# Kernel tuning notes

Measured on AMD Instinct MI355X. Metric: run time of the kernel, lower is better.

The kernel has to match this reference:

```python
import jax, jax.numpy as jnp
import numpy as np
from jax import lax

B, T = 16384, 10
H = 256
CAR_V, REG_V, POI_V, WEEK_V, TIME_V = 1000000, 100000, 1000, 7, 1440
LABELS = 500
IN = 39  # 16+8+4+3+8


def _lstm_layer(x, Wih, Whh, bih, bhh):
    # x: [B, T, D] -> outputs [B, T, H]; PyTorch gate order i,f,g,o
    b = x.shape[0]
    h0 = jnp.zeros((b, H), x.dtype)
    c0 = jnp.zeros((b, H), x.dtype)
    # Precompute input projections for all timesteps in one GEMM
    xg = jnp.einsum('btd,gd->btg', x, Wih) + bih + bhh  # [B, T, 4H]

    def step(carry, xt_g):
        h, c = carry
        gates = xt_g + h @ Whh.T  # [B, 4H]
        i, f, g, o = jnp.split(gates, 4, axis=-1)
        i, f, o = jax.nn.sigmoid(i), jax.nn.sigmoid(f), jax.nn.sigmoid(o)
        g = jnp.tanh(g)
        c = f * c + i * g
        h = o * jnp.tanh(c)
        return (h, c), h

    _, ys = lax.scan(step, (h0, c0), xg.transpose(1, 0, 2))  # ys: [T, B, H]
    return ys.transpose(1, 0, 2)


def setup_inputs() -> dict:
    key = jax.random.key(0)
    ks = jax.random.split(key, 20)
    s = 0.05
    return {
        'car_idx': jax.random.randint(ks[0], (B, T), 0, CAR_V),
        'region_idx': jax.random.randint(ks[1], (B, T), 0, REG_V),
        'poi_idx': jax.random.randint(ks[2], (B, T), 0, POI_V),
        'week_idx': jax.random.randint(ks[3], (B, T), 0, WEEK_V),
        'time_idx': jax.random.randint(ks[4], (B, T), 0, TIME_V),
        'car_emb': jax.random.normal(ks[5], (CAR_V, 16), jnp.float32) * s,
        'region_emb': jax.random.normal(ks[6], (REG_V, 8), jnp.float32) * s,
        'poi_emb': jax.random.normal(ks[7], (POI_V, 4), jnp.float32) * s,
        'week_emb': jax.random.normal(ks[8], (WEEK_V, 3), jnp.float32) * s,
        'time_emb': jax.random.normal(ks[9], (TIME_V, 8), jnp.float32) * s,
        'Wih0': jax.random.normal(ks[10], (4 * H, IN), jnp.float32) * s,
        'Whh0': jax.random.normal(ks[11], (4 * H, H), jnp.float32) * s,
        'bih0': jax.random.normal(ks[12], (4 * H,), jnp.float32) * s,
        'bhh0': jax.random.normal(ks[13], (4 * H,), jnp.float32) * s,
        'Wih1': jax.random.normal(ks[14], (4 * H, H), jnp.float32) * s,
        'Whh1': jax.random.normal(ks[15], (4 * H, H), jnp.float32) * s,
        'bih1': jax.random.normal(ks[16], (4 * H,), jnp.float32) * s,
        'bhh1': jax.random.normal(ks[17], (4 * H,), jnp.float32) * s,
        'Wout': jax.random.normal(ks[18], (LABELS, H), jnp.float32) * s,
        'bout': jax.random.normal(ks[19], (LABELS,), jnp.float32) * s,
    }


def reference(car_idx, region_idx, poi_idx, week_idx, time_idx,
              car_emb, region_emb, poi_emb, week_emb, time_emb,
              Wih0, Whh0, bih0, bhh0, Wih1, Whh1, bih1, bhh1,
              Wout, bout):
    # Batched version of the original per-item embedding-lookup + concat loop
    x = jnp.concatenate([
        car_emb[car_idx],      # [B, T, 16]
        region_emb[region_idx],  # [B, T, 8]
        poi_emb[poi_idx],      # [B, T, 4]
        week_emb[week_idx],    # [B, T, 3]
        time_emb[time_idx],    # [B, T, 8]
    ], axis=-1)  # [B, T, 39]
    h1 = _lstm_layer(x, Wih0, Whh0, bih0, bhh0)
    h2 = _lstm_layer(h1, Wih1, Whh1, bih1, bhh1)
    return h2[:, -1, :] @ Wout.T + bout  # [B, LABELS]
```

## Files before the change

### kernel.cpp

```cpp
#include <hip/hip_runtime.h>
#include <hip/hip_bf16.h>

#define BB 16384
#define TT 10
#define NLAB 500

typedef __attribute__((ext_vector_type(8))) __bf16 bf16x8;
typedef __attribute__((ext_vector_type(4))) float f32x4;
typedef __attribute__((ext_vector_type(8))) short short8v;

__device__ __forceinline__ unsigned short f2bf(float f) {
  union { float f; unsigned int u; } x; x.f = f;
  unsigned int r = 0x7fffu + ((x.u >> 16) & 1u);
  return (unsigned short)((x.u + r) >> 16);
}

__device__ __forceinline__ float sigm(float x) {
  return __builtin_amdgcn_rcpf(1.f + __builtin_amdgcn_exp2f(-1.4426950408889634f * x));
}
__device__ __forceinline__ float tanh_(float x) {
  float ax = fabsf(x);
  float e = __builtin_amdgcn_exp2f(-2.8853900817779268f * ax);
  float r = (1.f - e) * __builtin_amdgcn_rcpf(1.f + e);
  return copysignf(r, x);
}

__device__ __forceinline__ void gload_lds16(const unsigned short* g, unsigned short* l) {
  __builtin_amdgcn_global_load_lds(
      (const __attribute__((address_space(1))) unsigned int*)g,
      (__attribute__((address_space(3))) unsigned int*)l, 16, 0, 0);
}

#define SCHED0() __builtin_amdgcn_sched_barrier(0)
#define BAR_LGKM()                                                       \
  { SCHED0(); asm volatile("s_waitcnt lgkmcnt(0)" ::: "memory");         \
    __builtin_amdgcn_s_barrier(); SCHED0(); }
#define BAR_LGKM_VM4()                                                   \
  { SCHED0(); asm volatile("s_waitcnt vmcnt(4) lgkmcnt(0)" ::: "memory");\
    __builtin_amdgcn_s_barrier(); SCHED0(); }

__global__ void prep_w(const float* __restrict__ Wih0, const float* __restrict__ Whh0,
                       const float* __restrict__ bih0, const float* __restrict__ bhh0,
                       const float* __restrict__ Wih1, const float* __restrict__ Whh1,
                       const float* __restrict__ bih1, const float* __restrict__ bhh1,
                       const float* __restrict__ Wout, const float* __restrict__ bout,
                       unsigned short* __restrict__ wall, float* __restrict__ bblob) {
  int i = blockIdx.x * 256 + threadIdx.x;
  if (i < 983040) {
    int c = i >> 14, r = i & 16383;
    int wid = r >> 11, frag = (r >> 9) & 3, lane = (r >> 3) & 63, e = r & 7;
    int kin = ((lane >> 4) << 3) + e;
    float v;
    if (c < 20) {
      int pass = c / 10, ks = c % 10;
      int n = (pass * 2 + (frag >> 1)) * 256 + wid * 32 + (frag & 1) * 16 + (lane & 15);
      int k = ks * 32 + kin;
      if (k < 64) v = (k < 39) ? Wih0[n * 39 + k] : 0.f;
      else        v = Whh0[n * 256 + (k - 64)];
    } else if (c < 52) {
      int idx = c - 20;
      int pass = idx >> 4, half = (idx >> 3) & 1, ks = idx & 7;
      int n = (pass * 2 + (frag >> 1)) * 256 + wid * 32 + (frag & 1) * 16 + (lane & 15);
      int k = ks * 32 + kin;
      v = half ? Wih1[n * 256 + k]
               : Whh1[n * 256 + k];
    } else {
      int ks = c - 52;
      int n = wid * 64 + frag * 16 + (lane & 15);
      int k = ks * 32 + kin;
      v = (n < NLAB) ? Wout[n * 256 + k] : 0.f;
    }
    wall[i] = f2bf(v);
  } else {
    int j = i - 983040;
    if (j < 1024)       bblob[j] = bih0[j] + bhh0[j];
    else if (j < 2048)  bblob[j] = bih1[j - 1024] + bhh1[j - 1024];
    else if (j < 2560) { int n = j - 2048; bblob[j] = (n < NLAB) ? bout[n] : 0.f; }
  }
}

__global__ void gather_x(const int* __restrict__ car_idx, const int* __restrict__ region_idx,
                         const int* __restrict__ poi_idx, const int* __restrict__ week_idx,
                         const int* __restrict__ time_idx,
                         const float* __restrict__ car_emb, const float* __restrict__ region_emb,
                         const float* __restrict__ poi_emb, const float* __restrict__ week_emb,
                         const float* __restrict__ time_emb,
                         unsigned short* __restrict__ xfrag) {
  int tid = blockIdx.x * 256 + threadIdx.x;
  if (tid >= BB * TT) return;
  int t = tid / BB;
  int b = tid - t * BB;
  int ii = b * TT + t;
  float v[64];
#pragma unroll
  for (int k = 0; k < 64; ++k) v[k] = 0.f;
  { const float* p = car_emb + (size_t)car_idx[ii] * 16;
#pragma unroll
    for (int k = 0; k < 16; ++k) v[k] = p[k]; }
  { const float* p = region_emb + (size_t)region_idx[ii] * 8;
#pragma unroll
    for (int k = 0; k < 8; ++k) v[16 + k] = p[k]; }
  { const float* p = poi_emb + (size_t)poi_idx[ii] * 4;
#pragma unroll
    for (int k = 0; k < 4; ++k) v[24 + k] = p[k]; }
  { const float* p = week_emb + (size_t)week_idx[ii] * 3;
#pragma unroll
    for (int k = 0; k < 3; ++k) v[28 + k] = p[k]; }
  { const float* p = time_emb + (size_t)time_idx[ii] * 8;
#pragma unroll
    for (int k = 0; k < 8; ++k) v[31 + k] = p[k]; }

  int tile = b >> 6, rb = (b >> 4) & 3, lrow = b & 15;
  size_t base = ((size_t)tile * TT + t) * 4096;
#pragma unroll
  for (int c = 0; c < 8; ++c) {
    int kc = c >> 2;
    int lane = lrow + ((c & 3) << 4);
    size_t off = base + (size_t)((((kc << 2) + rb) << 6) + lane) * 8;
    short8v s;
#pragma unroll
    for (int e = 0; e < 8; ++e) s[e] = (short)f2bf(v[c * 8 + e]);
    *(short8v*)(xfrag + off) = s;
  }
}

__device__ __forceinline__ f32x4 MF(bf16x8 a, bf16x8 b, f32x4 c) {
  return __builtin_amdgcn_mfma_f32_16x16x32_bf16(a, b, c, 0, 0, 0);
}

template <int NKS, int SPLIT>
__device__ __forceinline__ void gemm_pass(f32x4 (&acc)[2][2][4], bf16x8 (&bc)[4],
    const unsigned short* wp, const unsigned short* wnext,
    const unsigned short* ab1, const unsigned short* ab2, int lane) {
#define AADDR(KS) \
  ((SPLIT < NKS && (KS) >= SPLIT) ? (ab2 + ((KS) - SPLIT) * 2048) : (ab1 + (KS) * 2048))
  bf16x8 aA[4], aB[4];
  {
    const unsigned short* a0 = AADDR(0);
#pragma unroll
    for (int rb = 0; rb < 4; ++rb) aA[rb] = *(const bf16x8*)(a0 + rb * 512 + lane * 8);
  }
#pragma unroll 1
  for (int ks = 0; ks < NKS; ks += 2) {
    bf16x8 bn[4], b2[4];
    const unsigned short* w1 = wp + 16384;
#pragma unroll
    for (int f = 0; f < 4; ++f) bn[f] = *(const bf16x8*)(w1 + f * 512);
    const unsigned short* w2 = (ks + 2 < NKS) ? (wp + 32768) : wnext;
#pragma unroll
    for (int f = 0; f < 4; ++f) b2[f] = *(const bf16x8*)(w2 + f * 512);
    const unsigned short* an = AADDR(ks + 1);
#pragma unroll
    for (int rb = 0; rb < 4; ++rb) aB[rb] = *(const bf16x8*)(an + rb * 512 + lane * 8);
#pragma unroll
    for (int gl = 0; gl < 2; ++gl)
#pragma unroll
      for (int nb = 0; nb < 2; ++nb)
#pragma unroll
        for (int rb = 0; rb < 4; ++rb)
          acc[gl][nb][rb] = MF(aA[rb], bc[gl * 2 + nb], acc[gl][nb][rb]);
    const unsigned short* an2 = AADDR((ks + 2 < NKS) ? (ks + 2) : (NKS - 1));
#pragma unroll
    for (int rb = 0; rb < 4; ++rb) aA[rb] = *(const bf16x8*)(an2 + rb * 512 + lane * 8);
#pragma unroll
    for (int gl = 0; gl < 2; ++gl)
#pragma unroll
      for (int nb = 0; nb < 2; ++nb)
#pragma unroll
        for (int rb = 0; rb < 4; ++rb)
          acc[gl][nb][rb] = MF(aB[rb], bn[gl * 2 + nb], acc[gl][nb][rb]);
#pragma unroll
    for (int f = 0; f < 4; ++f) bc[f] = b2[f];
    wp += 32768;
  }
#undef AADDR
}

__device__ __forceinline__ void partial_if(f32x4 (&acc)[2][2][4], f32x4 (&cst)[2][4],
                                           float* sib) {
#pragma unroll
  for (int nb = 0; nb < 2; ++nb)
#pragma unroll
    for (int rb = 0; rb < 4; ++rb)
#pragma unroll
      for (int r = 0; r < 4; ++r) {
        sib[((nb << 4) + (rb << 2) + r) << 6] = sigm(acc[0][nb][rb][r]);
        cst[nb][rb][r] = sigm(acc[1][nb][rb][r]) * cst[nb][rb][r];
      }
}

__device__ __forceinline__ void finish_go(f32x4 (&acc)[2][2][4], f32x4 (&cst)[2][4],
    const float* sib, unsigned short* hbuf, int lane, int wid) {
  int lrow = ((lane >> 4) << 2);
  int l15 = lane & 15;
#pragma unroll
  for (int nb = 0; nb < 2; ++nb) {
    int jw = (nb << 4) + l15;
    int lane_dst_base = ((jw >> 3) << 4);
    int elem = jw & 7;
#pragma unroll
    for (int rb = 0; rb < 4; ++rb)
#pragma unroll
      for (int r = 0; r < 4; ++r) {
        float g = tanh_(acc[0][nb][rb][r]);
        float o = sigm(acc[1][nb][rb][r]);
        float c = cst[nb][rb][r] + sib[((nb << 4) + (rb << 2) + r) << 6] * g;
        cst[nb][rb][r] = c;
        float h = o * tanh_(c);
        int lane_dst = lrow + r + lane_dst_base;
        hbuf[(size_t)((((wid << 2) + rb) << 6) + lane_dst) * 8 + elem] = f2bf(h);
      }
  }
}

__global__ __launch_bounds__(512, 1) void lstm_fused(
    const unsigned short* __restrict__ xfrag, const unsigned short* __restrict__ wall,
    const float* __restrict__ bblob, float* __restrict__ out) {
  __shared__ __align__(16) unsigned short h1s[16384];
  __shared__ __align__(16) unsigned short h2s[16384];
  __shared__ __align__(16) unsigned short xts[4096];
  __shared__ __align__(16) float bls[2560];
  __shared__ __align__(16) float sis[16384];

  int tid = threadIdx.x, lane = tid & 63, wid = tid >> 6;
  int tile = blockIdx.x, b0 = tile << 6, l15 = lane & 15;

  { short8v z = {0, 0, 0, 0, 0, 0, 0, 0};
    short8v* p1 = (short8v*)h1s; short8v* p2 = (short8v*)h2s;
    for (int i = tid; i < 2048; i += 512) { p1[i] = z; p2[i] = z; } }
  for (int i = tid; i < 2560; i += 512) bls[i] = bblob[i];
  gload_lds16(xfrag + (size_t)(tile * TT) * 4096 + wid * 512 + lane * 8, xts + wid * 512);

  float* sib = sis + (wid << 11) + lane;

  const unsigned short* wb = wall + wid * 2048 + lane * 8;

  bf16x8 bc[4];
#pragma unroll
  for (int f = 0; f < 4; ++f) bc[f] = *(const bf16x8*)(wb + f * 512);

  asm volatile("s_waitcnt vmcnt(0)" ::: "memory");
  __syncthreads();

  f32x4 c1[2][4], c2[2][4];
#pragma unroll
  for (int nb = 0; nb < 2; ++nb)
#pragma unroll
    for (int rb = 0; rb < 4; ++rb) {
      c1[nb][rb] = (f32x4){0.f, 0.f, 0.f, 0.f};
      c2[nb][rb] = (f32x4){0.f, 0.f, 0.f, 0.f};
    }
  f32x4 acc[2][2][4];

#define ACC_BIAS(BOFF, GBASE)                                                     \
  _Pragma("unroll")                                                               \
  for (int gl = 0; gl < 2; ++gl)                                                  \
    _Pragma("unroll")                                                             \
    for (int nb = 0; nb < 2; ++nb) {                                              \
      float bv = bls[(BOFF) + (((GBASE) + gl) << 8) + (wid << 5) + (nb << 4) + l15]; \
      _Pragma("unroll")                                                           \
      for (int rb = 0; rb < 4; ++rb) acc[gl][nb][rb] = (f32x4){bv, bv, bv, bv};   \
    }

#pragma unroll 1
  for (int t = 0; t < TT; ++t) {
    ACC_BIAS(0, 0)
    gemm_pass<10, 2>(acc, bc, wb, wb + 163840, xts, h1s, lane);
    partial_if(acc, c1, sib);
    ACC_BIAS(0, 2)
    gemm_pass<10, 2>(acc, bc, wb + 163840, wb + 327680, xts, h1s, lane);
    BAR_LGKM()
    if (t < TT - 1)
      gload_lds16(xfrag + (size_t)(tile * TT + t + 1) * 4096 + wid * 512 + lane * 8,
                  xts + wid * 512);
    finish_go(acc, c1, sib, h1s, lane, wid);
    ACC_BIAS(1024, 0)
    gemm_pass<8, 8>(acc, bc, wb + 327680, wb + 458752, h2s, h2s, lane);
    BAR_LGKM()
    gemm_pass<8, 8>(acc, bc, wb + 458752, wb + 589824, h1s, h1s, lane);
    partial_if(acc, c2, sib);
    ACC_BIAS(1024, 2)
    gemm_pass<8, 8>(acc, bc, wb + 589824, wb + 720896, h2s, h2s, lane);
    gemm_pass<8, 8>(acc, bc, wb + 720896,
                    (t < TT - 1) ? wb : (wb + 851968), h1s, h1s, lane);
    BAR_LGKM_VM4()
    finish_go(acc, c2, sib, h2s, lane, wid);
  }
  BAR_LGKM()

#pragma unroll
  for (int gl = 0; gl < 2; ++gl)
#pragma unroll
    for (int nb = 0; nb < 2; ++nb) {
      float bv = bls[2048 + (wid << 6) + ((gl * 2 + nb) << 4) + l15];
#pragma unroll
      for (int rb = 0; rb < 4; ++rb) acc[gl][nb][rb] = (f32x4){bv, bv, bv, bv};
    }
  gemm_pass<8, 8>(acc, bc, wb + 851968, wb + 851968, h2s, h2s, lane);

#pragma unroll
  for (int gl = 0; gl < 2; ++gl)
#pragma unroll
    for (int nb = 0; nb < 2; ++nb) {
      int n = (wid << 6) + ((gl * 2 + nb) << 4) + l15;
      if (n < NLAB) {
#pragma unroll
        for (int rb = 0; rb < 4; ++rb)
#pragma unroll
          for (int r = 0; r < 4; ++r) {
            int row = (rb << 4) + ((lane >> 4) << 2) + r;
            out[(size_t)(b0 + row) * NLAB + n] = acc[gl][nb][rb][r];
          }
      }
    }
#undef ACC_BIAS
}

extern "C" void kernel_launch(void* const* d_in, const int* in_sizes, int n_in,
                              void* d_out, int out_size, void* d_ws, size_t ws_size,
                              hipStream_t stream) {
  const int* car_idx    = (const int*)d_in[0];
  const int* region_idx = (const int*)d_in[1];
  const int* poi_idx    = (const int*)d_in[2];
  const int* week_idx   = (const int*)d_in[3];
  const int* time_idx   = (const int*)d_in[4];
  const float* car_emb    = (const float*)d_in[5];
  const float* region_emb = (const float*)d_in[6];
  const float* poi_emb    = (const float*)d_in[7];
  const float* week_emb   = (const float*)d_in[8];
  const float* time_emb   = (const float*)d_in[9];
  const float* Wih0 = (const float*)d_in[10];
  const float* Whh0 = (const float*)d_in[11];
  const float* bih0 = (const float*)d_in[12];
  const float* bhh0 = (const float*)d_in[13];
  const float* Wih1 = (const float*)d_in[14];
  const float* Whh1 = (const float*)d_in[15];
  const float* bih1 = (const float*)d_in[16];
  const float* bhh1 = (const float*)d_in[17];
  const float* Wout = (const float*)d_in[18];
  const float* bout = (const float*)d_in[19];

  unsigned short* xfrag = (unsigned short*)d_ws;
  unsigned short* wallp = xfrag + 10485760;
  float* bblob = (float*)(wallp + 983040);

  prep_w<<<3850, 256, 0, stream>>>(Wih0, Whh0, bih0, bhh0, Wih1, Whh1, bih1, bhh1,
                                   Wout, bout, wallp, bblob);
  gather_x<<<640, 256, 0, stream>>>(car_idx, region_idx, poi_idx, week_idx, time_idx,
                                    car_emb, region_emb, poi_emb, week_emb, time_emb, xfrag);
  lstm_fused<<<256, 512, 0, stream>>>(xfrag, wallp, bblob, (float*)d_out);
}
```

Measured before the change: 299.0 us.

## Peel first timestep to skip zero-state recurrent GEMMs and tune MFMA scheduling

Peels timestep zero out of the loop. Since h1 and h2 start at zero, it runs only the input-projection GEMMs there, which skips the recurrent Whh work and the LDS zero-initialisation. The change also merges two layer-2 gate passes into one 16-step pass, loads the next B fragments directly into bc instead of through a temporary to save registers, and wraps the MFMA blocks in s_setprio. tanh is simplified to 2*sigmoid(2x)-1, which drops the abs/copysign but may overflow or lose precision for large negative inputs.

```diff
diff --git a/kernel.cpp b/kernel.cpp
--- a/kernel.cpp
+++ b/kernel.cpp
@@ -19,10 +19,8 @@
   return __builtin_amdgcn_rcpf(1.f + __builtin_amdgcn_exp2f(-1.4426950408889634f * x));
 }
 __device__ __forceinline__ float tanh_(float x) {
-  float ax = fabsf(x);
-  float e = __builtin_amdgcn_exp2f(-2.8853900817779268f * ax);
-  float r = (1.f - e) * __builtin_amdgcn_rcpf(1.f + e);
-  return copysignf(r, x);
+  float e = __builtin_amdgcn_exp2f(-2.8853900817779268f * x);
+  return 2.f * __builtin_amdgcn_rcpf(1.f + e) - 1.f;
 }
 
 __device__ __forceinline__ void gload_lds16(const unsigned short* g, unsigned short* l) {
@@ -142,16 +140,14 @@
   }
 #pragma unroll 1
   for (int ks = 0; ks < NKS; ks += 2) {
-    bf16x8 bn[4], b2[4];
+    bf16x8 bn[4];
     const unsigned short* w1 = wp + 16384;
 #pragma unroll
     for (int f = 0; f < 4; ++f) bn[f] = *(const bf16x8*)(w1 + f * 512);
-    const unsigned short* w2 = (ks + 2 < NKS) ? (wp + 32768) : wnext;
-#pragma unroll
-    for (int f = 0; f < 4; ++f) b2[f] = *(const bf16x8*)(w2 + f * 512);
     const unsigned short* an = AADDR(ks + 1);
 #pragma unroll
     for (int rb = 0; rb < 4; ++rb) aB[rb] = *(const bf16x8*)(an + rb * 512 + lane * 8);
+    __builtin_amdgcn_s_setprio(1);
 #pragma unroll
     for (int gl = 0; gl < 2; ++gl)
 #pragma unroll
@@ -159,9 +155,14 @@
 #pragma unroll
         for (int rb = 0; rb < 4; ++rb)
           acc[gl][nb][rb] = MF(aA[rb], bc[gl * 2 + nb], acc[gl][nb][rb]);
+    __builtin_amdgcn_s_setprio(0);
+    const unsigned short* w2 = (ks + 2 < NKS) ? (wp + 32768) : wnext;
+#pragma unroll
+    for (int f = 0; f < 4; ++f) bc[f] = *(const bf16x8*)(w2 + f * 512);
     const unsigned short* an2 = AADDR((ks + 2 < NKS) ? (ks + 2) : (NKS - 1));
 #pragma unroll
     for (int rb = 0; rb < 4; ++rb) aA[rb] = *(const bf16x8*)(an2 + rb * 512 + lane * 8);
+    __builtin_amdgcn_s_setprio(1);
 #pragma unroll
     for (int gl = 0; gl < 2; ++gl)
 #pragma unroll
@@ -169,8 +170,7 @@
 #pragma unroll
         for (int rb = 0; rb < 4; ++rb)
           acc[gl][nb][rb] = MF(aB[rb], bn[gl * 2 + nb], acc[gl][nb][rb]);
-#pragma unroll
-    for (int f = 0; f < 4; ++f) bc[f] = b2[f];
+    __builtin_amdgcn_s_setprio(0);
     wp += 32768;
   }
 #undef AADDR
@@ -225,9 +225,6 @@
   int tid = threadIdx.x, lane = tid & 63, wid = tid >> 6;
   int tile = blockIdx.x, b0 = tile << 6, l15 = lane & 15;
 
-  { short8v z = {0, 0, 0, 0, 0, 0, 0, 0};
-    short8v* p1 = (short8v*)h1s; short8v* p2 = (short8v*)h2s;
-    for (int i = tid; i < 2048; i += 512) { p1[i] = z; p2[i] = z; } }
   for (int i = tid; i < 2560; i += 512) bls[i] = bblob[i];
   gload_lds16(xfrag + (size_t)(tile * TT) * 4096 + wid * 512 + lane * 8, xts + wid * 512);
 
@@ -262,8 +259,26 @@
       for (int rb = 0; rb < 4; ++rb) acc[gl][nb][rb] = (f32x4){bv, bv, bv, bv};   \
     }
 
+  ACC_BIAS(0, 0)
+  gemm_pass<2, 2>(acc, bc, wb, wb + 163840, xts, xts, lane);
+  partial_if(acc, c1, sib);
+  ACC_BIAS(0, 2)
+  gemm_pass<2, 2>(acc, bc, wb + 163840, wb + 458752, xts, xts, lane);
+  BAR_LGKM()
+  gload_lds16(xfrag + (size_t)(tile * TT + 1) * 4096 + wid * 512 + lane * 8,
+              xts + wid * 512);
+  finish_go(acc, c1, sib, h1s, lane, wid);
+  ACC_BIAS(1024, 0)
+  BAR_LGKM()
+  gemm_pass<8, 8>(acc, bc, wb + 458752, wb + 720896, h1s, h1s, lane);
+  partial_if(acc, c2, sib);
+  ACC_BIAS(1024, 2)
+  gemm_pass<8, 8>(acc, bc, wb + 720896, wb, h1s, h1s, lane);
+  BAR_LGKM_VM4()
+  finish_go(acc, c2, sib, h2s, lane, wid);
+
 #pragma unroll 1
-  for (int t = 0; t < TT; ++t) {
+  for (int t = 1; t < TT; ++t) {
     ACC_BIAS(0, 0)
     gemm_pass<10, 2>(acc, bc, wb, wb + 163840, xts, h1s, lane);
     partial_if(acc, c1, sib);
@@ -280,9 +295,8 @@
     gemm_pass<8, 8>(acc, bc, wb + 458752, wb + 589824, h1s, h1s, lane);
     partial_if(acc, c2, sib);
     ACC_BIAS(1024, 2)
-    gemm_pass<8, 8>(acc, bc, wb + 589824, wb + 720896, h2s, h2s, lane);
-    gemm_pass<8, 8>(acc, bc, wb + 720896,
-                    (t < TT - 1) ? wb : (wb + 851968), h1s, h1s, lane);
+    gemm_pass<16, 8>(acc, bc, wb + 589824,
+                     (t < TT - 1) ? wb : (wb + 851968), h2s, h1s, lane);
     BAR_LGKM_VM4()
     finish_go(acc, c2, sib, h2s, lane, wid);
   }
```

Result: faster. 269.6 us (-9.9%).
